# Kernel optimization log

Measured on AMD Instinct MI355X. Metric: run time of the kernel, lower is better.

Reference implementation:

```python
import jax, jax.numpy as jnp
import numpy as np

N = 96        # num_nodes
D = 64        # emb_size / n_hid
BS = 16
T = 13
G = 1         # num_graph

# all N^2 ordered pairs, receiver-major: edge e=i*N+j has receiver i, sender j
_REC = jnp.repeat(jnp.arange(N), N)
_SEND = jnp.tile(jnp.arange(N), N)


def _lin(shape, key, scale=0.05):
    return (jax.random.normal(key, shape, dtype=jnp.float32) * scale)


def setup_inputs() -> dict:
    key = jax.random.key(0)
    ks = jax.random.split(key, 24)
    inp = {
        "skill_seq": jax.random.randint(ks[0], (BS, T), 0, N, dtype=jnp.int32),
        "adj": jax.random.uniform(ks[1], (G, BS, N, N), dtype=jnp.float32),
        "node_embeddings": jax.random.normal(ks[2], (G, N, D), dtype=jnp.float32),
        # edge MLP
        "W_msg1": _lin((2 * D, D), ks[3]), "b_msg1": jnp.zeros((D,), jnp.float32),
        "W_msg2": _lin((D, D), ks[4]),     "b_msg2": jnp.zeros((D,), jnp.float32),
        # GRU hidden projections (no bias)
        "W_hr": _lin((D, D), ks[5]), "W_hi": _lin((D, D), ks[6]), "W_hh": _lin((D, D), ks[7]),
        # GRU input projections (bias)
        "W_ir": _lin((D, D), ks[8]),  "b_ir": jnp.zeros((D,), jnp.float32),
        "W_ii": _lin((D, D), ks[9]),  "b_ii": jnp.zeros((D,), jnp.float32),
        "W_in": _lin((D, D), ks[10]), "b_in": jnp.zeros((D,), jnp.float32),
        # output MLP
        "W_o1": _lin((D, D), ks[11]), "b_o1": jnp.zeros((D,), jnp.float32),
        "W_o2": _lin((D, D), ks[12]), "b_o2": jnp.zeros((D,), jnp.float32),
        "W_o3": _lin((D, D), ks[13]), "b_o3": jnp.zeros((D,), jnp.float32),
    }
    return inp


def _forward(skill_seq, adj, node_embeddings,
             W_msg1, b_msg1, W_msg2, b_msg2,
             W_hr, W_hi, W_hh,
             W_ir, b_ir, W_ii, b_ii, W_in, b_in,
             W_o1, b_o1, W_o2, b_o2, W_o3, b_o3):
    bs, time_steps = skill_seq.shape
    hidden0 = jnp.zeros((G, bs, N, D), dtype=adj.dtype)
    emb = node_embeddings[0]  # [N, D] (num_graph=1)

    def step(hidden, skill_t):
        # gather senders/receivers over the node axis -> [G, bs, N^2, 2D]
        senders = hidden[:, :, _SEND, :]
        receivers = hidden[:, :, _REC, :]
        pre_msg = jnp.concatenate([senders, receivers], axis=-1)
        msg = jnp.tanh(pre_msg @ W_msg1 + b_msg1)        # [G, bs, N^2, D]
        msg = jnp.tanh(msg @ W_msg2 + b_msg2)
        msg = msg.reshape(G, bs, N, N, D)                # receiver i, sender j
        # mask by adjacency and scatter-sum over senders, then /N
        agg = jnp.einsum('gbij,gbijd->gbid', adj, msg) / N   # [G, bs, N, D]
        inputs = emb[skill_t][None, :, None, :]          # [1, bs, 1, D]
        r = jax.nn.sigmoid(inputs @ W_ir + b_ir + agg @ W_hr)
        i = jax.nn.sigmoid(inputs @ W_ii + b_ii + agg @ W_hi)
        n = jnp.tanh(inputs @ W_in + b_in + r * (agg @ W_hh))
        hidden = (1.0 - i) * n + i * hidden
        pred = jax.nn.relu(hidden @ W_o1 + b_o1)
        pred = jax.nn.relu(pred @ W_o2 + b_o2)
        pred = pred @ W_o3 + b_o3                        # [G, bs, N, D]
        return hidden, pred

    skills_t = skill_seq[:, :time_steps - 1].T           # [T-1, bs]
    _, preds = jax.lax.scan(step, hidden0, skills_t)     # [T-1, G, bs, N, D]
    # torch: stack(dim=1) -> [G, T-1, bs, N, D]; transpose(1,2) -> [G, bs, T-1, N, D]
    return jnp.transpose(preds, (1, 2, 0, 3, 4))


def reference(skill_seq, adj, node_embeddings,
              W_msg1, b_msg1, W_msg2, b_msg2,
              W_hr, W_hi, W_hh,
              W_ir, b_ir, W_ii, b_ii, W_in, b_in,
              W_o1, b_o1, W_o2, b_o2, W_o3, b_o3):
    return _forward(skill_seq, adj, node_embeddings,
                    W_msg1, b_msg1, W_msg2, b_msg2,
                    W_hr, W_hi, W_hh,
                    W_ir, b_ir, W_ii, b_ii, W_in, b_in,
                    W_o1, b_o1, W_o2, b_o2, W_o3, b_o3)
```

## Files before the change

kernel.cpp:

```cpp
#include <hip/hip_runtime.h>

typedef unsigned short ushort_t;
typedef __attribute__((ext_vector_type(8))) short short8;
typedef __attribute__((ext_vector_type(4))) float floatx4;

#define NN 96
#define DD 64
#define BSZ 16
#define TSTEP 12
#define JSPLIT 8
#define JPW 12
#define ITILES 6

#define OFF_HID   0u
#define OFF_S     393216u
#define OFF_R     786432u
#define OFF_E     1179648u
#define OFF_PART  1253376u
#define OFF_WSWZ  4399104u

static __device__ __forceinline__ short f2bf(float f){
    union { float f; unsigned u; } v; v.f = f;
    unsigned u = v.u;
    u += 0x7fffu + ((u >> 16) & 1u);
    return (short)(u >> 16);
}
static __device__ __forceinline__ float fast_tanh(float x){
    x = fminf(20.f, fmaxf(-20.f, x));
    float p = __expf(2.f * x);
    return (p - 1.f) * __builtin_amdgcn_rcpf(p + 1.f);
}
static __device__ __forceinline__ float fast_sigmoid(float x){
    x = fminf(30.f, fmaxf(-30.f, x));
    float p = __expf(-x);
    return __builtin_amdgcn_rcpf(1.f + p);
}
static __device__ __forceinline__ void zero4(floatx4* a){
    floatx4 z = {0.f,0.f,0.f,0.f};
    a[0]=z; a[1]=z; a[2]=z; a[3]=z;
}
static __device__ __forceinline__ void buildA(const float* sM, int col, int quad, short8& a0, short8& a1){
    floatx4 f0 = *(const floatx4*)&sM[col*68 + quad*8];
    floatx4 f1 = *(const floatx4*)&sM[col*68 + quad*8 + 4];
    floatx4 f2 = *(const floatx4*)&sM[col*68 + 32 + quad*8];
    floatx4 f3 = *(const floatx4*)&sM[col*68 + 32 + quad*8 + 4];
    #pragma unroll
    for (int jj = 0; jj < 4; jj++){
        a0[jj]   = f2bf(f0[jj]);
        a0[4+jj] = f2bf(f1[jj]);
        a1[jj]   = f2bf(f2[jj]);
        a1[4+jj] = f2bf(f3[jj]);
    }
}
static __device__ __forceinline__ void mm16(short8 a0, short8 a1, const short8* wzm, int l, floatx4* acc){
    #pragma unroll
    for (int nt = 0; nt < 4; nt++){
        short8 b0 = wzm[nt*64 + l];
        short8 b1 = wzm[(4 + nt)*64 + l];
        acc[nt] = __builtin_amdgcn_mfma_f32_16x16x32_bf16(a0, b0, acc[nt], 0, 0, 0);
        acc[nt] = __builtin_amdgcn_mfma_f32_16x16x32_bf16(a1, b1, acc[nt], 0, 0, 0);
    }
}

__global__ __launch_bounds__(256) void k_init(
    const float* __restrict__ emb, const float* __restrict__ Wmsg1,
    const float* __restrict__ Wmsg2,
    const float* __restrict__ Whr, const float* __restrict__ Whi, const float* __restrict__ Whh,
    const float* __restrict__ Wir, const float* __restrict__ bir,
    const float* __restrict__ Wii, const float* __restrict__ bii,
    const float* __restrict__ Win, const float* __restrict__ bin,
    const float* __restrict__ Wo1, const float* __restrict__ Wo2, const float* __restrict__ Wo3,
    float* __restrict__ wsf, float* __restrict__ Ef, ushort_t* __restrict__ wswz)
{
    int wg = blockIdx.x, tid = threadIdx.x;
    if (wg < 288) {
        floatx4 z = {0.f,0.f,0.f,0.f};
        ((floatx4*)wsf)[wg*256 + tid] = z;
    } else if (wg < 360) {
        int flat = (wg - 288)*256 + tid;
        int m = flat / 6144; int r = flat % 6144; int s = r >> 6; int d = r & 63;
        const float* W = (m==0)? Wir : (m==1)? Wii : Win;
        const float* B = (m==0)? bir : (m==1)? bii : bin;
        float acc = B[d];
        #pragma unroll 8
        for (int k = 0; k < 64; k++)
            acc += emb[s*64 + k] * W[k*64 + d];
        Ef[flat] = acc;
    } else {
        int flat = (wg - 360)*256 + tid;
        int m = flat >> 12; int q = flat & 4095;
        int jj = q & 7, lane = (q >> 3) & 63, nt = (q >> 9) & 3, kc = q >> 11;
        int k = kc*32 + ((lane >> 4) << 3) + jj;
        int n = nt*16 + (lane & 15);
        const float* src; int idx = k*64 + n;
        switch (m) {
          case 0: src = Wmsg2; break;
          case 1: src = Whr;  break;
          case 2: src = Whi;  break;
          case 3: src = Whh;  break;
          case 4: src = Wmsg1; break;
          case 5: src = Wmsg1; idx = (64 + k)*64 + n; break;
          case 6: src = Wo1; break;
          case 7: src = Wo2; break;
          default: src = Wo3; break;
        }
        wswz[flat] = (ushort_t)f2bf(src[idx]);
    }
}

__global__ __launch_bounds__(256) void k_msg(
    const float* __restrict__ adj, const float* __restrict__ b1in, const float* __restrict__ b2in,
    const float* __restrict__ Sg, const float* __restrict__ Rg,
    const ushort_t* __restrict__ wswz, float* __restrict__ partial)
{
    __shared__ float sS[JPW*64];
    __shared__ float sRB[16*68];
    __shared__ float sAdj[16*JPW];
    __shared__ float sAgg[4][16*68];
    int wg = blockIdx.x;
    int js = wg / 96; int rem = wg % 96; int b = rem / 6; int it = rem % 6;
    int tid = threadIdx.x; int w = tid >> 6; int l = tid & 63;
    int quad = l >> 4, col = l & 15;
    int j0 = js * JPW;

    for (int q = tid; q < JPW*16; q += 256) {
        int row = q >> 4, c4 = (q & 15) * 4;
        *(floatx4*)&sS[row*64 + c4] = *(const floatx4*)&Sg[(b*NN + j0 + row)*64 + c4];
    }
    for (int q = tid; q < 16*16; q += 256) {
        int row = q >> 4, c4 = (q & 15) * 4;
        floatx4 r4 = *(const floatx4*)&Rg[(b*NN + it*16 + row)*64 + c4];
        floatx4 b4 = *(const floatx4*)&b1in[c4];
        floatx4 o = r4 + b4;
        *(floatx4*)&sRB[row*68 + c4] = o;
    }
    for (int q = tid; q < 16*JPW; q += 256) {
        int i = q / JPW, j = q % JPW;
        sAdj[q] = adj[(b*NN + it*16 + i)*NN + j0 + j];
    }
    const short8* wz = (const short8*)wswz;
    short8 w2f[2][4];
    #pragma unroll
    for (int kc = 0; kc < 2; kc++)
      #pragma unroll
      for (int nt = 0; nt < 4; nt++)
        w2f[kc][nt] = wz[(kc*4 + nt)*64 + l];
    float b2v[4];
    #pragma unroll
    for (int nt = 0; nt < 4; nt++) b2v[nt] = b2in[nt*16 + col];
    __syncthreads();

    float rbv[16];
    #pragma unroll
    for (int c = 0; c < 4; c++)
        *(floatx4*)&rbv[c*4] = *(const floatx4*)&sRB[col*68 + (c>>1)*32 + quad*8 + (c&1)*4];

    float agg[4][4];
    #pragma unroll
    for (int nt=0;nt<4;nt++)
      #pragma unroll
      for (int r=0;r<4;r++) agg[nt][r] = 0.f;

    for (int c = 0; c < 3; c++) {
        int jl = w*3 + c;
        float sv[16];
        #pragma unroll
        for (int cc = 0; cc < 4; cc++)
            *(floatx4*)&sv[cc*4] = *(const floatx4*)&sS[jl*64 + (cc>>1)*32 + quad*8 + (cc&1)*4];
        short8 a0, a1;
        #pragma unroll
        for (int e = 0; e < 8; e++) {
            a0[e] = f2bf(fast_tanh(sv[e]   + rbv[e]));
            a1[e] = f2bf(fast_tanh(sv[8+e] + rbv[8+e]));
        }
        floatx4 acc[4];
        zero4(acc);
        #pragma unroll
        for (int nt = 0; nt < 4; nt++) {
            acc[nt] = __builtin_amdgcn_mfma_f32_16x16x32_bf16(a0, w2f[0][nt], acc[nt], 0,0,0);
            acc[nt] = __builtin_amdgcn_mfma_f32_16x16x32_bf16(a1, w2f[1][nt], acc[nt], 0,0,0);
        }
        float adjv[4];
        #pragma unroll
        for (int r = 0; r < 4; r++) adjv[r] = sAdj[(quad*4 + r)*JPW + jl];
        #pragma unroll
        for (int nt = 0; nt < 4; nt++)
          #pragma unroll
          for (int r = 0; r < 4; r++)
            agg[nt][r] += adjv[r] * fast_tanh(acc[nt][r] + b2v[nt]);
    }
    #pragma unroll
    for (int nt = 0; nt < 4; nt++)
      #pragma unroll
      for (int r = 0; r < 4; r++)
        sAgg[w][(quad*4 + r)*68 + nt*16 + col] = agg[nt][r];
    __syncthreads();
    {
        int i = tid >> 4, k4 = (tid & 15) * 4;
        floatx4 s0 = *(const floatx4*)&sAgg[0][i*68 + k4];
        floatx4 s1 = *(const floatx4*)&sAgg[1][i*68 + k4];
        floatx4 s2 = *(const floatx4*)&sAgg[2][i*68 + k4];
        floatx4 s3 = *(const floatx4*)&sAgg[3][i*68 + k4];
        floatx4 o = (s0 + s1) + (s2 + s3);
        o = o * (1.f/96.f);
        *(floatx4*)&partial[((js*BSZ + b)*NN + it*16 + i)*64 + k4] = o;
    }
}

__global__ __launch_bounds__(64) void k_gru(
    const int* __restrict__ skills, const float* __restrict__ partial,
    const float* __restrict__ Ef, const ushort_t* __restrict__ wswz,
    const float* __restrict__ bo1, const float* __restrict__ bo2, const float* __restrict__ bo3,
    float* __restrict__ hidden, float* __restrict__ Sg, float* __restrict__ Rg,
    float* __restrict__ out, int t)
{
    __shared__ float sM[16*68];
    int wg = blockIdx.x; int b = wg / 6, it = wg % 6;
    int l = threadIdx.x; int quad = l >> 4, col = l & 15;
    {
        int i = l >> 2, k4 = (l & 3) * 16;
        floatx4 a[4];
        zero4(a);
        for (int p = 0; p < JSPLIT; p++) {
            const float* base = &partial[((p*BSZ + b)*NN + it*16 + i)*64 + k4];
            #pragma unroll
            for (int cc = 0; cc < 4; cc++)
                a[cc] += *(const floatx4*)&base[cc*4];
        }
        #pragma unroll
        for (int cc = 0; cc < 4; cc++)
            *(floatx4*)&sM[i*68 + k4 + cc*4] = a[cc];
    }
    __syncthreads();
    short8 aggA0, aggA1;
    buildA(sM, col, quad, aggA0, aggA1);

    floatx4 Ar[4], Ai[4], Ah[4];
    zero4(Ar); zero4(Ai); zero4(Ah);
    mm16(aggA0, aggA1, (const short8*)wswz + 1*512, l, Ar);
    mm16(aggA0, aggA1, (const short8*)wswz + 2*512, l, Ai);
    mm16(aggA0, aggA1, (const short8*)wswz + 3*512, l, Ah);

    int s = skills[b*13 + t];
    const float* Er = Ef + 0*6144 + s*64;
    const float* Ei = Ef + 1*6144 + s*64;
    const float* En = Ef + 2*6144 + s*64;

    float hnew[4][4];
    #pragma unroll
    for (int nt = 0; nt < 4; nt++) {
      #pragma unroll
      for (int r = 0; r < 4; r++) {
        int d = nt*16 + col;
        int row = it*16 + quad*4 + r;
        float gr = fast_sigmoid(Er[d] + Ar[nt][r]);
        float gi = fast_sigmoid(Ei[d] + Ai[nt][r]);
        float nn = fast_tanh(En[d] + gr * Ah[nt][r]);
        float hold = hidden[(b*NN + row)*64 + d];
        float h = (1.f - gi)*nn + gi*hold;
        hidden[(b*NN + row)*64 + d] = h;
        hnew[nt][r] = h;
      }
    }
    __syncthreads();
    #pragma unroll
    for (int nt = 0; nt < 4; nt++)
      #pragma unroll
      for (int r = 0; r < 4; r++)
        sM[(quad*4 + r)*68 + nt*16 + col] = hnew[nt][r];
    __syncthreads();
    short8 hA0, hA1;
    buildA(sM, col, quad, hA0, hA1);

    floatx4 Sa[4], Ra[4];
    zero4(Sa); zero4(Ra);
    mm16(hA0, hA1, (const short8*)wswz + 4*512, l, Sa);
    mm16(hA0, hA1, (const short8*)wswz + 5*512, l, Ra);
    #pragma unroll
    for (int nt = 0; nt < 4; nt++)
      #pragma unroll
      for (int r = 0; r < 4; r++) {
        int d = nt*16 + col;
        int row = it*16 + quad*4 + r;
        Sg[(b*NN + row)*64 + d] = Sa[nt][r];
        Rg[(b*NN + row)*64 + d] = Ra[nt][r];
      }

    floatx4 O1[4]; zero4(O1);
    mm16(hA0, hA1, (const short8*)wswz + 6*512, l, O1);
    __syncthreads();
    #pragma unroll
    for (int nt = 0; nt < 4; nt++)
      #pragma unroll
      for (int r = 0; r < 4; r++)
        sM[(quad*4 + r)*68 + nt*16 + col] = fmaxf(0.f, O1[nt][r] + bo1[nt*16 + col]);
    __syncthreads();
    short8 p1A0, p1A1; buildA(sM, col, quad, p1A0, p1A1);
    floatx4 O2[4]; zero4(O2);
    mm16(p1A0, p1A1, (const short8*)wswz + 7*512, l, O2);
    __syncthreads();
    #pragma unroll
    for (int nt = 0; nt < 4; nt++)
      #pragma unroll
      for (int r = 0; r < 4; r++)
        sM[(quad*4 + r)*68 + nt*16 + col] = fmaxf(0.f, O2[nt][r] + bo2[nt*16 + col]);
    __syncthreads();
    short8 p2A0, p2A1; buildA(sM, col, quad, p2A0, p2A1);
    floatx4 O3[4]; zero4(O3);
    mm16(p2A0, p2A1, (const short8*)wswz + 8*512, l, O3);
    #pragma unroll
    for (int nt = 0; nt < 4; nt++)
      #pragma unroll
      for (int r = 0; r < 4; r++) {
        int d = nt*16 + col;
        int row = quad*4 + r;
        float v = O3[nt][r] + bo3[d];
        out[((b*TSTEP + t)*NN + it*16 + row)*64 + d] = v;
      }
}

extern "C" void kernel_launch(void* const* d_in, const int* in_sizes, int n_in,
                              void* d_out, int out_size, void* d_ws, size_t ws_size,
                              hipStream_t stream) {
    const int*   skills = (const int*)d_in[0];
    const float* adj    = (const float*)d_in[1];
    const float* emb    = (const float*)d_in[2];
    const float* Wmsg1  = (const float*)d_in[3];
    const float* b1     = (const float*)d_in[4];
    const float* Wmsg2  = (const float*)d_in[5];
    const float* b2     = (const float*)d_in[6];
    const float* Whr    = (const float*)d_in[7];
    const float* Whi    = (const float*)d_in[8];
    const float* Whh    = (const float*)d_in[9];
    const float* Wir    = (const float*)d_in[10];
    const float* bir    = (const float*)d_in[11];
    const float* Wii    = (const float*)d_in[12];
    const float* bii    = (const float*)d_in[13];
    const float* Win    = (const float*)d_in[14];
    const float* bin    = (const float*)d_in[15];
    const float* Wo1    = (const float*)d_in[16];
    const float* bo1    = (const float*)d_in[17];
    const float* Wo2    = (const float*)d_in[18];
    const float* bo2    = (const float*)d_in[19];
    const float* Wo3    = (const float*)d_in[20];
    const float* bo3    = (const float*)d_in[21];

    char* ws = (char*)d_ws;
    float*    hidden  = (float*)(ws + OFF_HID);
    float*    Sg      = (float*)(ws + OFF_S);
    float*    Rg      = (float*)(ws + OFF_R);
    float*    Ef      = (float*)(ws + OFF_E);
    float*    partial = (float*)(ws + OFF_PART);
    ushort_t* wswz    = (ushort_t*)(ws + OFF_WSWZ);
    float*    out     = (float*)d_out;

    k_init<<<dim3(504), dim3(256), 0, stream>>>(emb, Wmsg1, Wmsg2, Whr, Whi, Whh,
        Wir, bir, Wii, bii, Win, bin, Wo1, Wo2, Wo3, (float*)ws, Ef, wswz);

    for (int t = 0; t < TSTEP; t++) {
        k_msg<<<dim3(JSPLIT*BSZ*ITILES), dim3(256), 0, stream>>>(adj, b1, b2, Sg, Rg, wswz, partial);
        k_gru<<<dim3(BSZ*ITILES), dim3(64), 0, stream>>>(skills, partial, Ef, wswz,
            bo1, bo2, bo3, hidden, Sg, Rg, out, t);
    }
}
```

Baseline: 292.4 us.

## Fuse GRU update into message kernel with redundant recompute and double-buffered state

Merges the per-step GRU/output kernel into the message kernel. Each workgroup redundantly reduces the previous step's partial aggregates and recomputes the GRU update for the row tiles it needs, so the sender and receiver projections are built directly in shared memory. Hidden state and partials are double-buffered across steps, and a final small kernel handles the last step. This halves the number of launches and the low-occupancy 96-block GRU kernel, at the cost of redundant GRU math and extra partial reads in every workgroup.

```diff
diff --git a/kernel.cpp b/kernel.cpp
--- a/kernel.cpp
+++ b/kernel.cpp
@@ -12,12 +12,12 @@
 #define JPW 12
 #define ITILES 6
 
-#define OFF_HID   0u
-#define OFF_S     393216u
-#define OFF_R     786432u
-#define OFF_E     1179648u
-#define OFF_PART  1253376u
-#define OFF_WSWZ  4399104u
+#define OFF_H0    0u
+#define OFF_H1    393216u
+#define OFF_P0    786432u
+#define OFF_P1    3932160u
+#define OFF_E     7077888u
+#define OFF_WSWZ  7151616u
 
 static __device__ __forceinline__ short f2bf(float f){
     union { float f; unsigned u; } v; v.f = f;
@@ -70,14 +70,14 @@
     const float* __restrict__ Wii, const float* __restrict__ bii,
     const float* __restrict__ Win, const float* __restrict__ bin,
     const float* __restrict__ Wo1, const float* __restrict__ Wo2, const float* __restrict__ Wo3,
-    float* __restrict__ wsf, float* __restrict__ Ef, ushort_t* __restrict__ wswz)
+    float* __restrict__ H0, float* __restrict__ Ef, ushort_t* __restrict__ wswz)
 {
     int wg = blockIdx.x, tid = threadIdx.x;
-    if (wg < 288) {
+    if (wg < 96) {
         floatx4 z = {0.f,0.f,0.f,0.f};
-        ((floatx4*)wsf)[wg*256 + tid] = z;
-    } else if (wg < 360) {
-        int flat = (wg - 288)*256 + tid;
+        ((floatx4*)H0)[wg*256 + tid] = z;
+    } else if (wg < 168) {
+        int flat = (wg - 96)*256 + tid;
         int m = flat / 6144; int r = flat % 6144; int s = r >> 6; int d = r & 63;
         const float* W = (m==0)? Wir : (m==1)? Wii : Win;
         const float* B = (m==0)? bir : (m==1)? bii : bin;
@@ -87,7 +87,7 @@
             acc += emb[s*64 + k] * W[k*64 + d];
         Ef[flat] = acc;
     } else {
-        int flat = (wg - 360)*256 + tid;
+        int flat = (wg - 168)*256 + tid;
         int m = flat >> 12; int q = flat & 4095;
         int jj = q & 7, lane = (q >> 3) & 63, nt = (q >> 9) & 3, kc = q >> 11;
         int k = kc*32 + ((lane >> 4) << 3) + jj;
@@ -108,37 +108,32 @@
     }
 }
 
-__global__ __launch_bounds__(256) void k_msg(
-    const float* __restrict__ adj, const float* __restrict__ b1in, const float* __restrict__ b2in,
-    const float* __restrict__ Sg, const float* __restrict__ Rg,
-    const ushort_t* __restrict__ wswz, float* __restrict__ partial)
+__global__ __launch_bounds__(256, 3) void k_step(
+    const int* __restrict__ skills, const float* __restrict__ adj,
+    const float* __restrict__ b1in, const float* __restrict__ b2in,
+    const float* __restrict__ bo1, const float* __restrict__ bo2, const float* __restrict__ bo3,
+    const float* __restrict__ Ef, const ushort_t* __restrict__ wswz,
+    const float* __restrict__ Hprev, float* __restrict__ Hnext,
+    const float* __restrict__ Pprev, float* __restrict__ Pnext,
+    float* __restrict__ out, int t)
 {
     __shared__ float sS[JPW*64];
     __shared__ float sRB[16*68];
     __shared__ float sAdj[16*JPW];
     __shared__ float sAgg[4][16*68];
+    __shared__ float sMg[3][16*68];
+
     int wg = blockIdx.x;
     int js = wg / 96; int rem = wg % 96; int b = rem / 6; int it = rem % 6;
     int tid = threadIdx.x; int w = tid >> 6; int l = tid & 63;
     int quad = l >> 4, col = l & 15;
     int j0 = js * JPW;
-
-    for (int q = tid; q < JPW*16; q += 256) {
-        int row = q >> 4, c4 = (q & 15) * 4;
-        *(floatx4*)&sS[row*64 + c4] = *(const floatx4*)&Sg[(b*NN + j0 + row)*64 + c4];
-    }
-    for (int q = tid; q < 16*16; q += 256) {
-        int row = q >> 4, c4 = (q & 15) * 4;
-        floatx4 r4 = *(const floatx4*)&Rg[(b*NN + it*16 + row)*64 + c4];
-        floatx4 b4 = *(const floatx4*)&b1in[c4];
-        floatx4 o = r4 + b4;
-        *(floatx4*)&sRB[row*68 + c4] = o;
-    }
+    const short8* wz = (const short8*)wswz;
+
     for (int q = tid; q < 16*JPW; q += 256) {
         int i = q / JPW, j = q % JPW;
         sAdj[q] = adj[(b*NN + it*16 + i)*NN + j0 + j];
     }
-    const short8* wz = (const short8*)wswz;
     short8 w2f[2][4];
     #pragma unroll
     for (int kc = 0; kc < 2; kc++)
@@ -148,6 +143,91 @@
     float b2v[4];
     #pragma unroll
     for (int nt = 0; nt < 4; nt++) b2v[nt] = b2in[nt*16 + col];
+
+    int tau = (w == 0) ? it : (w == 1) ? (j0 >> 4) : ((j0 + 11) >> 4);
+    bool pa = (t > 0) && (w < 3);
+    if (pa) {
+        int i = l >> 2, k4 = (l & 3) * 16;
+        floatx4 a[4];
+        zero4(a);
+        for (int p = 0; p < JSPLIT; p++) {
+            const float* base = &Pprev[((p*BSZ + b)*NN + tau*16 + i)*64 + k4];
+            #pragma unroll
+            for (int cc = 0; cc < 4; cc++)
+                a[cc] += *(const floatx4*)&base[cc*4];
+        }
+        #pragma unroll
+        for (int cc = 0; cc < 4; cc++)
+            *(floatx4*)&sMg[w][i*68 + k4 + cc*4] = a[cc];
+    }
+    __syncthreads();
+    if (pa) {
+        short8 A0, A1;
+        buildA(sMg[w], col, quad, A0, A1);
+        floatx4 Ar[4], Ai[4], Ah[4];
+        zero4(Ar); zero4(Ai); zero4(Ah);
+        mm16(A0, A1, wz + 1*512, l, Ar);
+        mm16(A0, A1, wz + 2*512, l, Ai);
+        mm16(A0, A1, wz + 3*512, l, Ah);
+        int s = skills[b*13 + (t-1)];
+        const float* Er = Ef + 0*6144 + s*64;
+        const float* Ei = Ef + 1*6144 + s*64;
+        const float* En = Ef + 2*6144 + s*64;
+        #pragma unroll
+        for (int nt = 0; nt < 4; nt++) {
+          #pragma unroll
+          for (int r = 0; r < 4; r++) {
+            int d = nt*16 + col;
+            int row = tau*16 + quad*4 + r;
+            float gr = fast_sigmoid(Er[d] + Ar[nt][r]);
+            float gi = fast_sigmoid(Ei[d] + Ai[nt][r]);
+            float nn2 = fast_tanh(En[d] + gr * Ah[nt][r]);
+            float h = (1.f - gi)*nn2 + gi*Hprev[(b*NN + row)*64 + d];
+            if (js == 0 && w == 0) Hnext[(b*NN + row)*64 + d] = h;
+            sMg[w][(quad*4 + r)*68 + d] = h;
+          }
+        }
+    }
+    __syncthreads();
+    if (pa) {
+        short8 h0, h1;
+        buildA(sMg[w], col, quad, h0, h1);
+        if (w == 0) {
+            floatx4 Ra[4];
+            zero4(Ra);
+            mm16(h0, h1, wz + 5*512, l, Ra);
+            #pragma unroll
+            for (int nt = 0; nt < 4; nt++)
+              #pragma unroll
+              for (int r = 0; r < 4; r++) {
+                int d = nt*16 + col;
+                sRB[(quad*4 + r)*68 + d] = Ra[nt][r] + b1in[d];
+              }
+        } else {
+            floatx4 Sa[4];
+            zero4(Sa);
+            mm16(h0, h1, wz + 4*512, l, Sa);
+            #pragma unroll
+            for (int nt = 0; nt < 4; nt++)
+              #pragma unroll
+              for (int r = 0; r < 4; r++) {
+                int g = tau*16 + quad*4 + r;
+                if (g >= j0 && g < j0 + JPW)
+                    sS[(g - j0)*64 + nt*16 + col] = Sa[nt][r];
+              }
+        }
+    }
+    if (t == 0) {
+        for (int q = tid; q < JPW*16; q += 256) {
+            int row = q >> 4, c4 = (q & 15) * 4;
+            floatx4 z = {0.f,0.f,0.f,0.f};
+            *(floatx4*)&sS[row*64 + c4] = z;
+        }
+        for (int q = tid; q < 16*16; q += 256) {
+            int row = q >> 4, c4 = (q & 15) * 4;
+            *(floatx4*)&sRB[row*68 + c4] = *(const floatx4*)&b1in[c4];
+        }
+    }
     __syncthreads();
 
     float rbv[16];
@@ -203,20 +283,67 @@
         floatx4 s3 = *(const floatx4*)&sAgg[3][i*68 + k4];
         floatx4 o = (s0 + s1) + (s2 + s3);
         o = o * (1.f/96.f);
-        *(floatx4*)&partial[((js*BSZ + b)*NN + it*16 + i)*64 + k4] = o;
-    }
-}
-
-__global__ __launch_bounds__(64) void k_gru(
+        *(floatx4*)&Pnext[((js*BSZ + b)*NN + it*16 + i)*64 + k4] = o;
+    }
+
+    bool domlp = (js == 0 && w == 0 && t > 0);
+    __syncthreads();
+    {
+        short8 x0, x1; floatx4 O[4];
+        if (domlp) {
+            buildA(sMg[0], col, quad, x0, x1);
+            zero4(O);
+            mm16(x0, x1, wz + 6*512, l, O);
+            #pragma unroll
+            for (int nt = 0; nt < 4; nt++)
+              #pragma unroll
+              for (int r = 0; r < 4; r++)
+                sMg[0][(quad*4 + r)*68 + nt*16 + col] = fmaxf(0.f, O[nt][r] + bo1[nt*16 + col]);
+        }
+    }
+    __syncthreads();
+    {
+        short8 x0, x1; floatx4 O[4];
+        if (domlp) {
+            buildA(sMg[0], col, quad, x0, x1);
+            zero4(O);
+            mm16(x0, x1, wz + 7*512, l, O);
+            #pragma unroll
+            for (int nt = 0; nt < 4; nt++)
+              #pragma unroll
+              for (int r = 0; r < 4; r++)
+                sMg[0][(quad*4 + r)*68 + nt*16 + col] = fmaxf(0.f, O[nt][r] + bo2[nt*16 + col]);
+        }
+    }
+    __syncthreads();
+    {
+        short8 x0, x1; floatx4 O[4];
+        if (domlp) {
+            buildA(sMg[0], col, quad, x0, x1);
+            zero4(O);
+            mm16(x0, x1, wz + 8*512, l, O);
+            #pragma unroll
+            for (int nt = 0; nt < 4; nt++)
+              #pragma unroll
+              for (int r = 0; r < 4; r++) {
+                int d = nt*16 + col;
+                int row = quad*4 + r;
+                out[((b*TSTEP + (t-1))*NN + it*16 + row)*64 + d] = O[nt][r] + bo3[d];
+              }
+        }
+    }
+}
+
+__global__ __launch_bounds__(64) void k_fin(
     const int* __restrict__ skills, const float* __restrict__ partial,
     const float* __restrict__ Ef, const ushort_t* __restrict__ wswz,
     const float* __restrict__ bo1, const float* __restrict__ bo2, const float* __restrict__ bo3,
-    float* __restrict__ hidden, float* __restrict__ Sg, float* __restrict__ Rg,
-    float* __restrict__ out, int t)
+    const float* __restrict__ Hprev, float* __restrict__ out, int t)
 {
     __shared__ float sM[16*68];
     int wg = blockIdx.x; int b = wg / 6, it = wg % 6;
     int l = threadIdx.x; int quad = l >> 4, col = l & 15;
+    const short8* wz = (const short8*)wswz;
     {
         int i = l >> 2, k4 = (l & 3) * 16;
         floatx4 a[4];
@@ -232,21 +359,18 @@
             *(floatx4*)&sM[i*68 + k4 + cc*4] = a[cc];
     }
     __syncthreads();
-    short8 aggA0, aggA1;
-    buildA(sM, col, quad, aggA0, aggA1);
-
+    short8 A0, A1;
+    buildA(sM, col, quad, A0, A1);
     floatx4 Ar[4], Ai[4], Ah[4];
     zero4(Ar); zero4(Ai); zero4(Ah);
-    mm16(aggA0, aggA1, (const short8*)wswz + 1*512, l, Ar);
-    mm16(aggA0, aggA1, (const short8*)wswz + 2*512, l, Ai);
-    mm16(aggA0, aggA1, (const short8*)wswz + 3*512, l, Ah);
-
+    mm16(A0, A1, wz + 1*512, l, Ar);
+    mm16(A0, A1, wz + 2*512, l, Ai);
+    mm16(A0, A1, wz + 3*512, l, Ah);
     int s = skills[b*13 + t];
     const float* Er = Ef + 0*6144 + s*64;
     const float* Ei = Ef + 1*6144 + s*64;
     const float* En = Ef + 2*6144 + s*64;
-
-    float hnew[4][4];
+    __syncthreads();
     #pragma unroll
     for (int nt = 0; nt < 4; nt++) {
       #pragma unroll
@@ -255,39 +379,16 @@
         int row = it*16 + quad*4 + r;
         float gr = fast_sigmoid(Er[d] + Ar[nt][r]);
         float gi = fast_sigmoid(Ei[d] + Ai[nt][r]);
-        float nn = fast_tanh(En[d] + gr * Ah[nt][r]);
-        float hold = hidden[(b*NN + row)*64 + d];
-        float h = (1.f - gi)*nn + gi*hold;
-        hidden[(b*NN + row)*64 + d] = h;
-        hnew[nt][r] = h;
+        float nn2 = fast_tanh(En[d] + gr * Ah[nt][r]);
+        float h = (1.f - gi)*nn2 + gi*Hprev[(b*NN + row)*64 + d];
+        sM[(quad*4 + r)*68 + d] = h;
       }
     }
     __syncthreads();
-    #pragma unroll
-    for (int nt = 0; nt < 4; nt++)
-      #pragma unroll
-      for (int r = 0; r < 4; r++)
-        sM[(quad*4 + r)*68 + nt*16 + col] = hnew[nt][r];
-    __syncthreads();
-    short8 hA0, hA1;
-    buildA(sM, col, quad, hA0, hA1);
-
-    floatx4 Sa[4], Ra[4];
-    zero4(Sa); zero4(Ra);
-    mm16(hA0, hA1, (const short8*)wswz + 4*512, l, Sa);
-    mm16(hA0, hA1, (const short8*)wswz + 5*512, l, Ra);
-    #pragma unroll
-    for (int nt = 0; nt < 4; nt++)
-      #pragma unroll
-      for (int r = 0; r < 4; r++) {
-        int d = nt*16 + col;
-        int row = it*16 + quad*4 + r;
-        Sg[(b*NN + row)*64 + d] = Sa[nt][r];
-        Rg[(b*NN + row)*64 + d] = Ra[nt][r];
-      }
-
+    short8 h0, h1;
+    buildA(sM, col, quad, h0, h1);
     floatx4 O1[4]; zero4(O1);
-    mm16(hA0, hA1, (const short8*)wswz + 6*512, l, O1);
+    mm16(h0, h1, wz + 6*512, l, O1);
     __syncthreads();
     #pragma unroll
     for (int nt = 0; nt < 4; nt++)
@@ -297,7 +398,7 @@
     __syncthreads();
     short8 p1A0, p1A1; buildA(sM, col, quad, p1A0, p1A1);
     floatx4 O2[4]; zero4(O2);
-    mm16(p1A0, p1A1, (const short8*)wswz + 7*512, l, O2);
+    mm16(p1A0, p1A1, wz + 7*512, l, O2);
     __syncthreads();
     #pragma unroll
     for (int nt = 0; nt < 4; nt++)
@@ -307,15 +408,14 @@
     __syncthreads();
     short8 p2A0, p2A1; buildA(sM, col, quad, p2A0, p2A1);
     floatx4 O3[4]; zero4(O3);
-    mm16(p2A0, p2A1, (const short8*)wswz + 8*512, l, O3);
+    mm16(p2A0, p2A1, wz + 8*512, l, O3);
     #pragma unroll
     for (int nt = 0; nt < 4; nt++)
       #pragma unroll
       for (int r = 0; r < 4; r++) {
         int d = nt*16 + col;
         int row = quad*4 + r;
-        float v = O3[nt][r] + bo3[d];
-        out[((b*TSTEP + t)*NN + it*16 + row)*64 + d] = v;
+        out[((b*TSTEP + t)*NN + it*16 + row)*64 + d] = O3[nt][r] + bo3[d];
       }
 }
 
@@ -346,20 +446,20 @@
     const float* bo3    = (const float*)d_in[21];
 
     char* ws = (char*)d_ws;
-    float*    hidden  = (float*)(ws + OFF_HID);
-    float*    Sg      = (float*)(ws + OFF_S);
-    float*    Rg      = (float*)(ws + OFF_R);
+    float*    H[2] = { (float*)(ws + OFF_H0), (float*)(ws + OFF_H1) };
+    float*    P[2] = { (float*)(ws + OFF_P0), (float*)(ws + OFF_P1) };
     float*    Ef      = (float*)(ws + OFF_E);
-    float*    partial = (float*)(ws + OFF_PART);
     ushort_t* wswz    = (ushort_t*)(ws + OFF_WSWZ);
     float*    out     = (float*)d_out;
 
-    k_init<<<dim3(504), dim3(256), 0, stream>>>(emb, Wmsg1, Wmsg2, Whr, Whi, Whh,
-        Wir, bir, Wii, bii, Win, bin, Wo1, Wo2, Wo3, (float*)ws, Ef, wswz);
+    k_init<<<dim3(312), dim3(256), 0, stream>>>(emb, Wmsg1, Wmsg2, Whr, Whi, Whh,
+        Wir, bir, Wii, bii, Win, bin, Wo1, Wo2, Wo3, H[0], Ef, wswz);
 
     for (int t = 0; t < TSTEP; t++) {
-        k_msg<<<dim3(JSPLIT*BSZ*ITILES), dim3(256), 0, stream>>>(adj, b1, b2, Sg, Rg, wswz, partial);
-        k_gru<<<dim3(BSZ*ITILES), dim3(64), 0, stream>>>(skills, partial, Ef, wswz,
-            bo1, bo2, bo3, hidden, Sg, Rg, out, t);
-    }
-}
+        k_step<<<dim3(JSPLIT*BSZ*ITILES), dim3(256), 0, stream>>>(
+            skills, adj, b1, b2, bo1, bo2, bo3, Ef, wswz,
+            H[(t+1)&1], H[t&1], P[(t+1)&1], P[t&1], out, t);
+    }
+    k_fin<<<dim3(BSZ*ITILES), dim3(64), 0, stream>>>(skills, P[1], Ef, wswz,
+        bo1, bo2, bo3, H[1], out, TSTEP-1);
+}
```

Result: slower. 345.6 us (+18.2%).
